# Optimization experiments

Measured on AMD Instinct MI355X. Metric: run time of the kernel, lower is better.

The kernel has to match this reference:

```python
import jax, jax.numpy as jnp
import numpy as np

WINDOW = 25
DIM_HEAD = 32


def _rel_pos_indices(w):
    # replicates the torch buffer: grid of (i,j) positions, pairwise offsets
    pos = np.arange(w)
    gi, gj = np.meshgrid(pos, pos, indexing='ij')
    grid = np.stack([gi.reshape(-1), gj.reshape(-1)], axis=-1)  # (w*w, 2)
    rel = grid[:, None, :] - grid[None, :, :] + (w - 1)          # (n, n, 2)
    return jnp.asarray(rel[..., 0] * (2 * w - 1) + rel[..., 1], dtype=jnp.int32)


def setup_inputs() -> dict:
    key = jax.random.key(0)
    k1, k2, k3, k4 = jax.random.split(key, 4)
    b, d, w = 32, 256, WINDOW
    heads = d // DIM_HEAD
    x = jax.random.normal(k1, (b, d, w, w), dtype=jnp.float32)
    W_qkv = jax.random.normal(k2, (d, 3 * d), dtype=jnp.float32) * 0.02
    W_out = jax.random.normal(k3, (d, d), dtype=jnp.float32) * 0.02
    rel_emb = jax.random.normal(k4, ((2 * w - 1) ** 2, heads), dtype=jnp.float32) * 0.02
    return {"x": x, "W_qkv": W_qkv, "W_out": W_out, "rel_emb": rel_emb}


def reference(x, W_qkv, W_out, rel_emb):
    b, d, H, W = x.shape
    h = d // DIM_HEAD
    scale = DIM_HEAD ** -0.5
    n = H * W

    # b d H W -> b n d
    xf = x.reshape(b, d, n).transpose(0, 2, 1)
    qkv = xf @ W_qkv                       # (b, n, 3d); columns ordered q,k,v
    q, k, v = jnp.split(qkv, 3, axis=-1)

    def to_heads(t):
        return t.reshape(b, n, h, DIM_HEAD).transpose(0, 2, 1, 3)  # b h n dh

    q = to_heads(q) * scale
    k = to_heads(k)
    v = to_heads(v)

    sim = jnp.einsum('bhid,bhjd->bhij', q, k)          # (b, h, n, n)
    bias = rel_emb[_rel_pos_indices(H)]                # (n, n, h)
    sim = sim + bias.transpose(2, 0, 1)[None]          # add per-head bias
    attn = jax.nn.softmax(sim, axis=-1)

    out = jnp.einsum('bhij,bhjd->bhid', attn, v)       # (b, h, n, dh)
    # b m (H W) dh -> b H W (m dh)  (head-major channel concat)
    out = out.transpose(0, 2, 1, 3).reshape(b, H, W, d)
    out = out @ W_out                                  # output projection (no bias)
    return out.transpose(0, 3, 1, 2)                   # b d H W
```

## Files before the change

### kernel.cpp

```cpp
#include <hip/hip_runtime.h>
#include <hip/hip_bf16.h>
#include <cstdint>

typedef __bf16 bf16x8 __attribute__((ext_vector_type(8)));
typedef __bf16 bf16x4 __attribute__((ext_vector_type(4)));
typedef float  f32x4  __attribute__((ext_vector_type(4)));

__device__ __forceinline__ int div25(int v) { return (v * 1311) >> 15; }

#if __has_builtin(__builtin_amdgcn_exp2f)
__device__ __forceinline__ float fast_exp2(float x) { return __builtin_amdgcn_exp2f(x); }
#else
__device__ __forceinline__ float fast_exp2(float x) { return exp2f(x); }
#endif

__device__ __forceinline__ int sniff_isbf(const void* p)
{
    const unsigned short* x = (const unsigned short*)p;
    int cnt = 0;
    #pragma unroll
    for (int i = 0; i < 16; ++i) {
        int e = (x[2 * i] >> 7) & 0xFF;
        cnt += (e >= 90 && e <= 143) ? 1 : 0;
    }
    return cnt > 8;
}

__global__ __launch_bounds__(256) void k_pre(
    const void* __restrict__ x, const void* __restrict__ Wqkv,
    const void* __restrict__ Wout, const void* __restrict__ rel,
    __bf16* __restrict__ xT, __bf16* __restrict__ Wt, __bf16* __restrict__ WoT,
    __bf16* __restrict__ biasC)
{
    __shared__ float tile[64][65];
    int bid = blockIdx.x;
    if (bid < 1280) {
        int isbf = sniff_isbf(x);
        int b = bid / 40, rem = bid % 40;
        int c0 = (rem % 10) * 64, r0 = (rem / 10) * 64;
        const int R = 256, C = 625, Cpad = 640;
        int tc = threadIdx.x & 63, tg = threadIdx.x >> 6;
        const unsigned short* sb = (const unsigned short*)x + (size_t)b * (256 * 625);
        const float*          sf = (const float*)x          + (size_t)b * (256 * 625);
        #pragma unroll
        for (int rr = 0; rr < 16; ++rr) {
            int r = r0 + tg * 16 + rr, c = c0 + tc;
            float v = 0.f;
            if (r < R && c < C) {
                if (isbf) v = __uint_as_float((unsigned int)sb[r * C + c] << 16);
                else      v = sf[r * C + c];
            }
            tile[tg * 16 + rr][tc] = v;
        }
        __syncthreads();
        __bf16* d = xT + (size_t)b * (640 * 256);
        #pragma unroll
        for (int rr = 0; rr < 16; ++rr) {
            int c = c0 + tg * 16 + rr, r = r0 + tc;
            if (c < Cpad && r < R) d[(size_t)c * R + r] = (__bf16)tile[tc][tg * 16 + rr];
        }
    } else if (bid < 1344) {
        int q = bid - 1280;
        int bx = q % 16, by = q / 16;
        int isbf = sniff_isbf(Wqkv);
        int isqkv = (bx < 12);
        int bxx = isqkv ? bx : (bx - 12);
        const void* src = isqkv ? Wqkv : Wout;
        __bf16* dst = isqkv ? Wt : WoT;
        int R = 256, C = isqkv ? 768 : 256;
        int r0 = by * 64, c0 = bxx * 64;
        int tc = threadIdx.x & 63, tg = threadIdx.x >> 6;
        const unsigned short* sb = (const unsigned short*)src;
        const float*          sf = (const float*)src;
        #pragma unroll
        for (int rr = 0; rr < 16; ++rr) {
            int r = r0 + tg * 16 + rr, c = c0 + tc;
            float v;
            if (isbf) v = __uint_as_float((unsigned int)sb[r * C + c] << 16);
            else      v = sf[r * C + c];
            tile[tg * 16 + rr][tc] = v;
        }
        __syncthreads();
        const float qs = 0.25503494f;
        #pragma unroll
        for (int rr = 0; rr < 16; ++rr) {
            int c = c0 + tg * 16 + rr, r = r0 + tc;
            float v = tile[tc][tg * 16 + rr];
            if (isqkv && c < 256) v *= qs;
            dst[(size_t)c * R + r] = (__bf16)v;
        }
    } else {
        const float LOG2E = 1.4426950408889634f;
        int isbf = sniff_isbf(rel);
        int q = bid - 1344;
        int ig = q % 40, h = q / 40;
        for (int t0 = 0; t0 < 10; ++t0) {
            int t  = t0 * 256 + threadIdx.x;
            int jc = t >> 7;
            int js = (t >> 6) & 1;
            int ln = t & 63;
            int qd = ln >> 4, l = ln & 15;
            int i = ig * 16 + l;
            int di = div25(i), ri = i - 25 * di;
            bf16x4 out;
            #pragma unroll
            for (int rr = 0; rr < 4; ++rr) {
                int j = jc * 32 + js * 16 + qd * 4 + rr;
                float v;
                if (j >= 625) {
                    v = -43281.f;
                } else {
                    int dj = div25(j);
                    int idx = (di - dj + 24) * 49 + ri - (j - 25 * dj) + 24;
                    idx = min(max(idx, 0), 2400);
                    float r;
                    if (isbf) r = (float)((const __bf16*)rel)[idx * 8 + h];
                    else      r = ((const float*)rel)[idx * 8 + h];
                    v = r * LOG2E;
                }
                out[rr] = (__bf16)v;
            }
            *(bf16x4*)(biasC + ((size_t)(h * 40 + ig) * 20 + jc) * 512 + js * 256 + ln * 4) = out;
        }
    }
}

#define AS(r, c) pool[(size_t)(r) * 40 + (c)]
#define BS(r, c) pool[5120 + (size_t)(r) * 40 + (c)]
#define CS(r, c) pool[(size_t)(r) * 44 + (c)]
__global__ __launch_bounds__(256, 2) void k_qkv(
    const __bf16* __restrict__ xT,
    const __bf16* __restrict__ Wt,
    __bf16* __restrict__ Q,
    __bf16* __restrict__ Km,
    __bf16* __restrict__ Vt)
{
    __shared__ __align__(16) __bf16 pool[10240];
    int L = blockIdx.x;
    int xcd = L & 7;
    int cc  = L >> 3;
    int pairIdx = xcd * 20 + cc / 6;
    int jt = cc - (cc / 6) * 6;
    int b  = pairIdx / 5;
    int pt = pairIdx - b * 5;
    int p0 = pt * 128, j0 = jt * 128;
    int tid = threadIdx.x;
    int w = tid >> 6, lane = tid & 63;
    int quad = lane >> 4, l15 = lane & 15;
    int wr = w >> 1, wc = w & 1;

    int srow = tid >> 2, scg = (tid & 3) * 8;
    const __bf16* ag  = xT + ((size_t)(b * 640 + p0 + srow) * 256) + scg;
    const __bf16* ag2 = ag + 64 * 256;
    const __bf16* bg  = Wt + ((size_t)(j0 + srow) * 256) + scg;
    const __bf16* bg2 = bg + 64 * 256;

    f32x4 acc[4][4] = {};
    for (int kk = 0; kk < 8; ++kk) {
        int c0 = kk * 32;
        bf16x8 a0 = *(const bf16x8*)(ag + c0);
        bf16x8 a1 = *(const bf16x8*)(ag2 + c0);
        bf16x8 b0 = *(const bf16x8*)(bg + c0);
        bf16x8 b1 = *(const bf16x8*)(bg2 + c0);
        __syncthreads();
        *(bf16x8*)(&AS(srow, scg))      = a0;
        *(bf16x8*)(&AS(64 + srow, scg)) = a1;
        *(bf16x8*)(&BS(srow, scg))      = b0;
        *(bf16x8*)(&BS(64 + srow, scg)) = b1;
        __syncthreads();
        bf16x8 af[4], bfr[4];
        #pragma unroll
        for (int t = 0; t < 4; ++t) {
            af[t]  = *(const bf16x8*)(&AS(wr * 64 + t * 16 + l15, quad * 8));
            bfr[t] = *(const bf16x8*)(&BS(wc * 64 + t * 16 + l15, quad * 8));
        }
        #pragma unroll
        for (int i = 0; i < 4; ++i)
            #pragma unroll
            for (int j = 0; j < 4; ++j)
                acc[i][j] = __builtin_amdgcn_mfma_f32_16x16x32_bf16(af[i], bfr[j], acc[i][j], 0, 0, 0);
    }

    if (jt < 4) {
        for (int r = 0; r < 4; ++r) {
            __syncthreads();
            if (wc == (r >> 1)) {
                #pragma unroll
                for (int i = 0; i < 4; ++i) {
                    #pragma unroll
                    for (int js = 0; js < 2; ++js) {
                        int jp = (r & 1) * 2 + js;
                        int col = js * 16 + l15;
                        int prow = wr * 64 + i * 16 + quad * 4;
                        #pragma unroll
                        for (int rr = 0; rr < 4; ++rr)
                            CS(prow + rr, col) = (__bf16)acc[i][jp][rr];
                    }
                }
            }
            __syncthreads();
            int jj = j0 + r * 32;
            __bf16* dst; int hh;
            if (jj < 256) { hh = jj >> 5; dst = Q; }
            else          { hh = (jj - 256) >> 5; dst = Km; }
            int p = tid >> 1, d0 = (tid & 1) * 16;
            size_t base = ((size_t)((b * 8 + hh) * 640) + p0 + p) * 32 + d0;
            #pragma unroll
            for (int k4 = 0; k4 < 4; ++k4) {
                bf16x4 v4 = *(const bf16x4*)(&CS(p, d0 + k4 * 4));
                *(bf16x4*)(dst + base + k4 * 4) = v4;
            }
        }
    } else {
        #pragma unroll
        for (int i = 0; i < 4; ++i) {
            #pragma unroll
            for (int j = 0; j < 4; ++j) {
                int jj = j0 + wc * 64 + j * 16 + l15 - 512;
                int h = jj >> 5, t = jj & 31;
                int p = p0 + wr * 64 + i * 16 + quad * 4;
                bf16x4 vv;
                #pragma unroll
                for (int rr = 0; rr < 4; ++rr) vv[rr] = (__bf16)acc[i][j][rr];
                *(bf16x4*)(Vt + ((size_t)((b * 8 + h) * 32) + t) * 640 + p) = vv;
            }
        }
    }
}

__global__ __launch_bounds__(128, 3) void k_attn(
    const __bf16* __restrict__ Q,
    const __bf16* __restrict__ Km,
    const __bf16* __restrict__ Vt,
    const __bf16* __restrict__ biasC,
    __bf16* __restrict__ ctx)
{
    __shared__ __align__(16) __bf16 P[2][2][64][40];
    __shared__ float ssum[2][64];
    int bh = blockIdx.x, b = bh >> 3, h = bh & 7;
    int tid = threadIdx.x, w = tid >> 6, lane = tid & 63;
    int quad = lane >> 4, l15 = lane & 15;
    int i0 = (blockIdx.y * 2 + w) * 64;

    bf16x8 qa[4];
    #pragma unroll
    for (int m = 0; m < 4; ++m)
        qa[m] = *(const bf16x8*)(Q + ((size_t)bh * 640 + i0 + 16 * m + l15) * 32 + quad * 8);
    const __bf16* kbase = Km + (size_t)bh * 640 * 32 + quad * 8;
    const __bf16* vbase = Vt + ((size_t)bh * 32 + l15) * 640 + quad * 8;
    const __bf16* bcb   = biasC + (size_t)(h * 40 + (i0 >> 4)) * 10240 + lane * 4;

    f32x4 o[4][2] = {};
    float psum[4] = {0.f, 0.f, 0.f, 0.f};

    bf16x8 k0 = *(const bf16x8*)(kbase + (size_t)l15 * 32);
    bf16x8 k1 = *(const bf16x8*)(kbase + (size_t)(16 + l15) * 32);
    bf16x4 bc[4][2];
    #pragma unroll
    for (int m = 0; m < 4; ++m) {
        bc[m][0] = *(const bf16x4*)(bcb + m * 10240);
        bc[m][1] = *(const bf16x4*)(bcb + m * 10240 + 256);
    }
    bf16x8 vC0 = {}, vC1 = {};

    for (int c = 0; c < 20; ++c) {
        int buf = c & 1;
        f32x4 s[4][2];
        __builtin_amdgcn_s_setprio(1);
        #pragma unroll
        for (int m = 0; m < 4; ++m) {
            f32x4 f0, f1;
            #pragma unroll
            for (int rr = 0; rr < 4; ++rr) { f0[rr] = (float)bc[m][0][rr]; f1[rr] = (float)bc[m][1][rr]; }
            s[m][0] = __builtin_amdgcn_mfma_f32_16x16x32_bf16(k0, qa[m], f0, 0, 0, 0);
            s[m][1] = __builtin_amdgcn_mfma_f32_16x16x32_bf16(k1, qa[m], f1, 0, 0, 0);
        }
        __builtin_amdgcn_s_setprio(0);
        int cn = min(c + 1, 19);
        bf16x8 k0n = *(const bf16x8*)(kbase + (size_t)(cn * 32 + l15) * 32);
        bf16x8 k1n = *(const bf16x8*)(kbase + (size_t)(cn * 32 + 16 + l15) * 32);
        bf16x8 vN0 = *(const bf16x8*)(vbase + c * 32);
        bf16x8 vN1 = *(const bf16x8*)(vbase + (size_t)16 * 640 + c * 32);
        bf16x4 bn[4][2];
        #pragma unroll
        for (int m = 0; m < 4; ++m) {
            bn[m][0] = *(const bf16x4*)(bcb + m * 10240 + cn * 512);
            bn[m][1] = *(const bf16x4*)(bcb + m * 10240 + cn * 512 + 256);
        }
        bf16x4 pk[4][2];
        #pragma unroll
        for (int m = 0; m < 4; ++m) {
            #pragma unroll
            for (int rr = 0; rr < 4; ++rr) {
                float e0 = fast_exp2(s[m][0][rr]); psum[m] += e0; pk[m][0][rr] = (__bf16)e0;
                float e1 = fast_exp2(s[m][1][rr]); psum[m] += e1; pk[m][1][rr] = (__bf16)e1;
            }
        }
        if (c > 0) {
            __builtin_amdgcn_s_setprio(1);
            #pragma unroll
            for (int m = 0; m < 4; ++m) {
                bf16x8 pa = *(const bf16x8*)(&P[w][buf ^ 1][16 * m + l15][quad * 8]);
                o[m][0] = __builtin_amdgcn_mfma_f32_16x16x32_bf16(pa, vC0, o[m][0], 0, 0, 0);
                o[m][1] = __builtin_amdgcn_mfma_f32_16x16x32_bf16(pa, vC1, o[m][1], 0, 0, 0);
            }
            __builtin_amdgcn_s_setprio(0);
        }
        #pragma unroll
        for (int m = 0; m < 4; ++m) {
            *(bf16x4*)(&P[w][buf][16 * m + l15][quad * 4])      = pk[m][0];
            *(bf16x4*)(&P[w][buf][16 * m + l15][16 + quad * 4]) = pk[m][1];
        }
        k0 = k0n; k1 = k1n; vC0 = vN0; vC1 = vN1;
        #pragma unroll
        for (int m = 0; m < 4; ++m) { bc[m][0] = bn[m][0]; bc[m][1] = bn[m][1]; }
    }
    __builtin_amdgcn_s_setprio(1);
    #pragma unroll
    for (int m = 0; m < 4; ++m) {
        bf16x8 pa = *(const bf16x8*)(&P[w][1][16 * m + l15][quad * 8]);
        o[m][0] = __builtin_amdgcn_mfma_f32_16x16x32_bf16(pa, vC0, o[m][0], 0, 0, 0);
        o[m][1] = __builtin_amdgcn_mfma_f32_16x16x32_bf16(pa, vC1, o[m][1], 0, 0, 0);
    }
    __builtin_amdgcn_s_setprio(0);

    #pragma unroll
    for (int m = 0; m < 4; ++m) {
        psum[m] += __shfl_xor(psum[m], 16);
        psum[m] += __shfl_xor(psum[m], 32);
    }
    if (quad == 0)
        #pragma unroll
        for (int m = 0; m < 4; ++m) ssum[w][16 * m + l15] = psum[m];
    #pragma unroll
    for (int m = 0; m < 4; ++m) {
        #pragma unroll
        for (int rr = 0; rr < 4; ++rr) {
            int il = 16 * m + quad * 4 + rr;
            float inv = 1.f / ssum[w][il];
            size_t base = ((size_t)b * 640 + i0 + il) * 256 + h * 32;
            ctx[base + l15]      = (__bf16)(o[m][0][rr] * inv);
            ctx[base + 16 + l15] = (__bf16)(o[m][1][rr] * inv);
        }
    }
}

__global__ __launch_bounds__(256, 2) void k_outproj(
    const __bf16* __restrict__ ctx,
    const __bf16* __restrict__ WoT,
    const void* __restrict__ xorig,
    void* __restrict__ out)
{
    __shared__ __align__(16) __bf16 As2[64][40];
    __shared__ __align__(16) __bf16 Bs2[256][40];
    int isbf = sniff_isbf(xorig);
    int b = blockIdx.y, pt = blockIdx.x;
    int p0 = pt * 64;
    int tid = threadIdx.x, w = tid >> 6, lane = tid & 63;
    int quad = lane >> 4, l15 = lane & 15;
    int srow = tid >> 2, scg = (tid & 3) * 8;
    const __bf16* ag = ctx + ((size_t)(b * 640 + p0 + srow) * 256) + scg;
    const __bf16* bg = WoT + (size_t)srow * 256 + scg;

    f32x4 acc[4][4] = {};
    for (int kk = 0; kk < 8; ++kk) {
        int c0 = kk * 32;
        bf16x8 a0 = *(const bf16x8*)(ag + c0);
        bf16x8 b0 = *(const bf16x8*)(bg + c0);
        bf16x8 b1 = *(const bf16x8*)(bg + 64 * 256 + c0);
        bf16x8 b2 = *(const bf16x8*)(bg + 128 * 256 + c0);
        bf16x8 b3 = *(const bf16x8*)(bg + 192 * 256 + c0);
        __syncthreads();
        *(bf16x8*)(&As2[srow][scg])       = a0;
        *(bf16x8*)(&Bs2[srow][scg])       = b0;
        *(bf16x8*)(&Bs2[64 + srow][scg])  = b1;
        *(bf16x8*)(&Bs2[128 + srow][scg]) = b2;
        *(bf16x8*)(&Bs2[192 + srow][scg]) = b3;
        __syncthreads();
        bf16x8 af[4], bfr[4];
        #pragma unroll
        for (int t = 0; t < 4; ++t) {
            af[t]  = *(const bf16x8*)(&As2[t * 16 + l15][quad * 8]);
            bfr[t] = *(const bf16x8*)(&Bs2[w * 64 + t * 16 + l15][quad * 8]);
        }
        #pragma unroll
        for (int i = 0; i < 4; ++i)
            #pragma unroll
            for (int j = 0; j < 4; ++j)
                acc[i][j] = __builtin_amdgcn_mfma_f32_16x16x32_bf16(af[i], bfr[j], acc[i][j], 0, 0, 0);
    }
    __bf16* outb = (__bf16*)out;
    float*  outf = (float*)out;
    #pragma unroll
    for (int i = 0; i < 4; ++i) {
        #pragma unroll
        for (int j = 0; j < 4; ++j) {
            int co = w * 64 + j * 16 + l15;
            #pragma unroll
            for (int rr = 0; rr < 4; ++rr) {
                int p = p0 + i * 16 + quad * 4 + rr;
                if (p < 625) {
                    size_t o = ((size_t)(b * 256) + co) * 625 + p;
                    if (isbf) outb[o] = (__bf16)acc[i][j][rr];
                    else      outf[o] = acc[i][j][rr];
                }
            }
        }
    }
}

extern "C" void kernel_launch(void* const* d_in, const int* in_sizes, int n_in,
                              void* d_out, int out_size, void* d_ws, size_t ws_size,
                              hipStream_t stream)
{
    const void* x    = d_in[0];
    const void* Wqkv = d_in[1];
    const void* Wout = d_in[2];
    const void* rel  = d_in[3];

    __bf16* ws    = (__bf16*)d_ws;
    __bf16* xT    = ws;
    __bf16* Wt    = xT + 10485760;
    __bf16* WoT   = Wt + 196608;
    __bf16* Q     = WoT + 65536;
    __bf16* Km    = Q + 5242880;
    __bf16* Vt    = Km + 5242880;
    __bf16* biasC = Vt + 5242880;
    __bf16* ctx   = biasC + 3276800;

    k_pre<<<1664, 256, 0, stream>>>(x, Wqkv, Wout, rel, xT, Wt, WoT, biasC);
    k_qkv<<<dim3(960), 256, 0, stream>>>(xT, Wt, Q, Km, Vt);
    k_attn<<<dim3(256, 5), 128, 0, stream>>>(Q, Km, Vt, biasC, ctx);
    k_outproj<<<dim3(10, 32), 256, 0, stream>>>(ctx, WoT, x, d_out);
}
```

Baseline: 160.8 us.

## Use direct global-to-LDS loads in QKV GEMM and interleave bias layout for wide loads

```diff
diff --git a/kernel.cpp b/kernel.cpp
--- a/kernel.cpp
+++ b/kernel.cpp
@@ -13,6 +13,14 @@
 #else
 __device__ __forceinline__ float fast_exp2(float x) { return exp2f(x); }
 #endif
+
+__device__ __forceinline__ void gll16(const __bf16* g, __bf16* l)
+{
+    __builtin_amdgcn_global_load_lds(
+        (__attribute__((address_space(1))) void*)(g),
+        (__attribute__((address_space(3))) void*)(l),
+        16, 0, 0);
+}
 
 __device__ __forceinline__ int sniff_isbf(const void* p)
 {
@@ -120,13 +128,13 @@
                 }
                 out[rr] = (__bf16)v;
             }
-            *(bf16x4*)(biasC + ((size_t)(h * 40 + ig) * 20 + jc) * 512 + js * 256 + ln * 4) = out;
-        }
-    }
-}
-
-#define AS(r, c) pool[(size_t)(r) * 40 + (c)]
-#define BS(r, c) pool[5120 + (size_t)(r) * 40 + (c)]
+            *(bf16x4*)(biasC + ((size_t)(h * 40 + ig) * 20 + jc) * 512 + ln * 8 + js * 4) = out;
+        }
+    }
+}
+
+#define AS(r, c) pool[(size_t)(r) * 32 + (c)]
+#define BS(r, c) pool[4096 + (size_t)(r) * 32 + (c)]
 #define CS(r, c) pool[(size_t)(r) * 44 + (c)]
 __global__ __launch_bounds__(256, 2) void k_qkv(
     const __bf16* __restrict__ xT,
@@ -135,7 +143,7 @@
     __bf16* __restrict__ Km,
     __bf16* __restrict__ Vt)
 {
-    __shared__ __align__(16) __bf16 pool[10240];
+    __shared__ __align__(16) __bf16 pool[8192];
     int L = blockIdx.x;
     int xcd = L & 7;
     int cc  = L >> 3;
@@ -158,15 +166,11 @@
     f32x4 acc[4][4] = {};
     for (int kk = 0; kk < 8; ++kk) {
         int c0 = kk * 32;
-        bf16x8 a0 = *(const bf16x8*)(ag + c0);
-        bf16x8 a1 = *(const bf16x8*)(ag2 + c0);
-        bf16x8 b0 = *(const bf16x8*)(bg + c0);
-        bf16x8 b1 = *(const bf16x8*)(bg2 + c0);
-        __syncthreads();
-        *(bf16x8*)(&AS(srow, scg))      = a0;
-        *(bf16x8*)(&AS(64 + srow, scg)) = a1;
-        *(bf16x8*)(&BS(srow, scg))      = b0;
-        *(bf16x8*)(&BS(64 + srow, scg)) = b1;
+        __syncthreads();
+        gll16(ag  + c0, &AS(srow, scg));
+        gll16(ag2 + c0, &AS(64 + srow, scg));
+        gll16(bg  + c0, &BS(srow, scg));
+        gll16(bg2 + c0, &BS(64 + srow, scg));
         __syncthreads();
         bf16x8 af[4], bfr[4];
         #pragma unroll
@@ -235,7 +239,7 @@
     const __bf16* __restrict__ biasC,
     __bf16* __restrict__ ctx)
 {
-    __shared__ __align__(16) __bf16 P[2][2][64][40];
+    __shared__ __align__(16) __bf16 P[2][2][64][44];
     __shared__ float ssum[2][64];
     int bh = blockIdx.x, b = bh >> 3, h = bh & 7;
     int tid = threadIdx.x, w = tid >> 6, lane = tid & 63;
@@ -248,19 +252,17 @@
         qa[m] = *(const bf16x8*)(Q + ((size_t)bh * 640 + i0 + 16 * m + l15) * 32 + quad * 8);
     const __bf16* kbase = Km + (size_t)bh * 640 * 32 + quad * 8;
     const __bf16* vbase = Vt + ((size_t)bh * 32 + l15) * 640 + quad * 8;
-    const __bf16* bcb   = biasC + (size_t)(h * 40 + (i0 >> 4)) * 10240 + lane * 4;
+    const __bf16* bcb   = biasC + (size_t)(h * 40 + (i0 >> 4)) * 10240 + lane * 8;
 
     f32x4 o[4][2] = {};
     float psum[4] = {0.f, 0.f, 0.f, 0.f};
 
     bf16x8 k0 = *(const bf16x8*)(kbase + (size_t)l15 * 32);
     bf16x8 k1 = *(const bf16x8*)(kbase + (size_t)(16 + l15) * 32);
-    bf16x4 bc[4][2];
-    #pragma unroll
-    for (int m = 0; m < 4; ++m) {
-        bc[m][0] = *(const bf16x4*)(bcb + m * 10240);
-        bc[m][1] = *(const bf16x4*)(bcb + m * 10240 + 256);
-    }
+    bf16x8 bc[4];
+    #pragma unroll
+    for (int m = 0; m < 4; ++m)
+        bc[m] = *(const bf16x8*)(bcb + m * 10240);
     bf16x8 vC0 = {}, vC1 = {};
 
     for (int c = 0; c < 20; ++c) {
@@ -271,7 +273,7 @@
         for (int m = 0; m < 4; ++m) {
             f32x4 f0, f1;
             #pragma unroll
-            for (int rr = 0; rr < 4; ++rr) { f0[rr] = (float)bc[m][0][rr]; f1[rr] = (float)bc[m][1][rr]; }
+            for (int rr = 0; rr < 4; ++rr) { f0[rr] = (float)bc[m][rr]; f1[rr] = (float)bc[m][4 + rr]; }
             s[m][0] = __builtin_amdgcn_mfma_f32_16x16x32_bf16(k0, qa[m], f0, 0, 0, 0);
             s[m][1] = __builtin_amdgcn_mfma_f32_16x16x32_bf16(k1, qa[m], f1, 0, 0, 0);
         }
@@ -281,12 +283,10 @@
         bf16x8 k1n = *(const bf16x8*)(kbase + (size_t)(cn * 32 + 16 + l15) * 32);
         bf16x8 vN0 = *(const bf16x8*)(vbase + c * 32);
         bf16x8 vN1 = *(const bf16x8*)(vbase + (size_t)16 * 640 + c * 32);
-        bf16x4 bn[4][2];
-        #pragma unroll
-        for (int m = 0; m < 4; ++m) {
-            bn[m][0] = *(const bf16x4*)(bcb + m * 10240 + cn * 512);
-            bn[m][1] = *(const bf16x4*)(bcb + m * 10240 + cn * 512 + 256);
-        }
+        bf16x8 bn[4];
+        #pragma unroll
+        for (int m = 0; m < 4; ++m)
+            bn[m] = *(const bf16x8*)(bcb + m * 10240 + cn * 512);
         bf16x4 pk[4][2];
         #pragma unroll
         for (int m = 0; m < 4; ++m) {
@@ -313,7 +313,7 @@
         }
         k0 = k0n; k1 = k1n; vC0 = vN0; vC1 = vN1;
         #pragma unroll
-        for (int m = 0; m < 4; ++m) { bc[m][0] = bn[m][0]; bc[m][1] = bn[m][1]; }
+        for (int m = 0; m < 4; ++m) bc[m] = bn[m];
     }
     __builtin_amdgcn_s_setprio(1);
     #pragma unroll
```

Measured after the change: 157.4 us. 2.1% less time.
